# Performance work log

Hardware: AMD Instinct MI355X
Metric: run time of the kernel (lower is better)

Reference implementation:

```python
import jax, jax.numpy as jnp
import numpy as np

B, S, E = 2, 2048, 2048
H, KVH, D = 16, 4, 128
GROUPS = H // KVH
WINDOW = 1024
CAP = 50.0
ROPE_BASE = 10000.0
RMS_EPS = 1e-6
LN_EPS = 1e-5

def setup_inputs() -> dict:
    key = jax.random.key(0)
    ks = jax.random.split(key, 5)
    return {
        "x": jax.random.normal(ks[0], (B, S, E), jnp.float32),
        "Wq": jax.random.normal(ks[1], (E, E), jnp.float32) * (1.0 / np.sqrt(E)),
        "Wk": jax.random.normal(ks[2], (KVH * D, E), jnp.float32) * (1.0 / np.sqrt(E)),
        "Wv": jax.random.normal(ks[3], (KVH * D, E), jnp.float32) * (1.0 / np.sqrt(E)),
        "Wo": jax.random.normal(ks[4], (E, E), jnp.float32) * (1.0 / np.sqrt(E * H)),
        "q_norm_w": jnp.ones((D,), jnp.float32),
        "k_norm_w": jnp.ones((D,), jnp.float32),
        "ln_gamma": jnp.ones((E,), jnp.float32),
        "ln_beta": jnp.zeros((E,), jnp.float32),
    }

def _rmsnorm(t, w):
    # normalize over last (head) dim
    var = jnp.mean(jnp.square(t), axis=-1, keepdims=True)
    return t * jax.lax.rsqrt(var + RMS_EPS) * w

def _rope(t):
    # t: [B, h, S, D]; rotate-half RoPE
    half = D // 2
    inv_freq = 1.0 / (ROPE_BASE ** (jnp.arange(0, D, 2, dtype=jnp.float32) / D))  # [D/2]
    ang = jnp.arange(S, dtype=jnp.float32)[:, None] * inv_freq[None, :]  # [S, D/2]
    cos = jnp.concatenate([jnp.cos(ang), jnp.cos(ang)], axis=-1)  # [S, D]
    sin = jnp.concatenate([jnp.sin(ang), jnp.sin(ang)], axis=-1)
    t1, t2 = t[..., :half], t[..., half:]
    rot = jnp.concatenate([-t2, t1], axis=-1)
    return t * cos + rot * sin

def reference(x, Wq, Wk, Wv, Wo, q_norm_w, k_norm_w, ln_gamma, ln_beta):
    b, s, _ = x.shape
    q = (x @ Wq.T).reshape(b, s, H, D).transpose(0, 2, 1, 3)    # [B,H,S,D]
    k = (x @ Wk.T).reshape(b, s, KVH, D).transpose(0, 2, 1, 3)  # [B,KVH,S,D]
    v = (x @ Wv.T).reshape(b, s, KVH, D).transpose(0, 2, 1, 3)
    # QK-RMSNorm (Gemma/PaLM2 style), then RoPE
    q = _rope(_rmsnorm(q, q_norm_w))
    k = _rope(_rmsnorm(k, k_norm_w))
    # GQA: repeat KV heads to match query heads
    k = jnp.repeat(k, GROUPS, axis=1)  # [B,H,S,D]
    v = jnp.repeat(v, GROUPS, axis=1)
    scores = jnp.einsum('bhqd,bhkd->bhqk', q, k) / jnp.sqrt(jnp.asarray(D, x.dtype))
    # tanh logit softcap (Gemma2)
    scores = CAP * jnp.tanh(scores / CAP)
    # causal + sliding-window mask: attend to j with 0 <= i-j < WINDOW
    i = jnp.arange(s)[:, None]
    j = jnp.arange(s)[None, :]
    mask = (j <= i) & ((i - j) < WINDOW)  # [S,S]
    neg = jnp.finfo(scores.dtype).min
    scores = jnp.where(mask[None, None], scores, neg)
    attn = jax.nn.softmax(scores, axis=-1)
    out = jnp.einsum('bhqk,bhkd->bhqd', attn, v)  # [B,H,S,D]
    out = out.transpose(0, 2, 1, 3).reshape(b, s, E) @ Wo.T
    # residual + LayerNorm (post-norm)
    y = x + out
    mu = jnp.mean(y, axis=-1, keepdims=True)
    var = jnp.var(y, axis=-1, keepdims=True)
    return (y - mu) * jax.lax.rsqrt(var + LN_EPS) * ln_gamma + ln_beta
```

## Files before the change

kernel.cpp:

```cpp
#include <hip/hip_runtime.h>
#include <stdint.h>

typedef __attribute__((ext_vector_type(8))) short short8;
typedef __attribute__((ext_vector_type(4))) float f32x4;
typedef unsigned short u16;
typedef unsigned int u32;

#define NTOK 4096
#define E 2048
#define S 2048
#define NH 16
#define NKVH 4
#define HD 128
#define NQKV 3072

__device__ __forceinline__ float bf2f(u16 u) {
    return __uint_as_float(((u32)u) << 16);
}
__device__ __forceinline__ u16 f2bf(float f) {
    u32 u = __float_as_uint(f);
    u32 r = (u + 0x7fffu + ((u >> 16) & 1u)) >> 16;
    return (u16)r;
}
__device__ __forceinline__ void gload_lds16(const u16* g, u16* l) {
    __builtin_amdgcn_global_load_lds(
        (const __attribute__((address_space(1))) unsigned int*)(g),
        (__attribute__((address_space(3))) unsigned int*)(l), 16, 0, 0);
}

__global__ void cast5(const float* __restrict__ x, const float* __restrict__ wq,
                      const float* __restrict__ wk, const float* __restrict__ wv,
                      const float* __restrict__ wo,
                      u16* __restrict__ xb, u16* __restrict__ wqkvb,
                      u16* __restrict__ wob) {
    int i = blockIdx.x * 256 + threadIdx.x;
    const float* s; u16* d; int rel;
    if (i < 2097152)      { s = x;  d = xb;  rel = i; }
    else if (i < 3145728) { s = wq; d = wqkvb; rel = i - 2097152; }
    else if (i < 3407872) { s = wk; d = wqkvb + 4194304; rel = i - 3145728; }
    else if (i < 3670016) { s = wv; d = wqkvb + 5242880; rel = i - 3407872; }
    else                  { s = wo; d = wob; rel = i - 3670016; }
    float4 v = *(const float4*)(s + (size_t)rel * 4);
    ushort4 o;
    o.x = f2bf(v.x); o.y = f2bf(v.y); o.z = f2bf(v.z); o.w = f2bf(v.w);
    *(ushort4*)(d + (size_t)rel * 4) = o;
}

#define LADDR(row, ko) ((row) * 64 + ((ko) ^ (((row) & 7) << 3)))
#define GSB   __builtin_amdgcn_sched_barrier(0)
#define GBAR  __builtin_amdgcn_s_barrier()
#define LGKM0 do { asm volatile("s_waitcnt lgkmcnt(0)" ::: "memory"); GSB; } while (0)
#define MIDBAR do { GSB; GBAR; LGKM0; } while (0)
#define ENDBAR do { __builtin_amdgcn_s_setprio(0); GSB; GBAR; } while (0)

__device__ __forceinline__ void stage1(u16* lds, const u16* g, int row0,
                                       int kt, int K, int tid) {
    const int rr = tid >> 3;
    const int chunk = (tid & 7) ^ (rr & 7);
    gload_lds16(g + (size_t)(row0 + rr) * K + kt + chunk * 8,
                lds + (row0 + (tid >> 6) * 8) * 64);
}

__global__ __launch_bounds__(512, 2)
void gemm_qkv(const u16* __restrict__ A, const u16* __restrict__ Bt,
              float* __restrict__ C, int M, int N, int K) {
    __shared__ u16 As2[2 * 8192];
    __shared__ u16 Bs2[2 * 24576];
    const int tid = threadIdx.x;
    const int w = tid >> 6, lane = tid & 63;
    const int lr = lane & 15, quad = lane >> 4;
    const int qo = quad * 8;
    const int wr = w >> 2, wc = w & 3;
    const int am = wr * 64;
    const int bn = wc * 96;

    const int nbx = N / 384;
    int wg = blockIdx.x;
    {
        const int nwg = gridDim.x;
        const int q = nwg >> 3, r = nwg & 7;
        const int xcd = wg & 7, loc = wg >> 3;
        wg = (xcd < r ? xcd * (q + 1) : r * (q + 1) + (xcd - r) * q) + loc;
    }
    const int n0 = (wg % nbx) * 384;
    const int m0 = (wg / nbx) * 128;

    const u16* gA = A + (size_t)m0 * K;
    const u16* gB = Bt + (size_t)n0 * K;
    const int nt = K >> 6;

    f32x4 acc[4][6];
#pragma unroll
    for (int mi = 0; mi < 4; mi++)
#pragma unroll
        for (int ni = 0; ni < 6; ni++)
            acc[mi][ni] = (f32x4){0.f, 0.f, 0.f, 0.f};

    short8 af[4][2], bf[6][2];

    stage1(As2, gA, 0, 0, K, tid);
    stage1(As2, gA, 64, 0, K, tid);
#pragma unroll
    for (int r = 0; r < 6; r++) stage1(Bs2, gB, r * 64, 0, K, tid);
    if (nt > 1) {
        stage1(As2 + 8192, gA, 0, 64, K, tid);
        stage1(As2 + 8192, gA, 64, 64, K, tid);
#pragma unroll
        for (int r = 0; r < 4; r++) stage1(Bs2 + 24576, gB, r * 64, 64, K, tid);
        asm volatile("s_waitcnt vmcnt(6)" ::: "memory");
    } else {
        asm volatile("s_waitcnt vmcnt(0)" ::: "memory");
    }
    GSB; GBAR;

    for (int t = 0; t < nt; ++t) {
        const int pb = t & 1;
        u16* Ap = As2 + pb * 8192;
        u16* Bp = Bs2 + pb * 24576;
        u16* Bn = Bs2 + (pb ^ 1) * 24576;
        const int kt1 = (t + 1) << 6, kt2 = (t + 2) << 6;

#pragma unroll
        for (int mi = 0; mi < 4; mi++)
#pragma unroll
            for (int kk = 0; kk < 2; kk++)
                af[mi][kk] = *(const short8*)&Ap[LADDR(am + mi * 16 + lr, kk * 32 + qo)];
#pragma unroll
        for (int ni = 0; ni < 3; ni++)
#pragma unroll
            for (int kk = 0; kk < 2; kk++)
                bf[ni][kk] = *(const short8*)&Bp[LADDR(bn + ni * 16 + lr, kk * 32 + qo)];
        if (t + 1 < nt) {
            stage1(Bn, gB, 256, kt1, K, tid);
            stage1(Bn, gB, 320, kt1, K, tid);
        }
        MIDBAR;
        __builtin_amdgcn_s_setprio(1);
#pragma unroll
        for (int mi = 0; mi < 2; mi++)
#pragma unroll
            for (int ni = 0; ni < 3; ni++)
#pragma unroll
                for (int kk = 0; kk < 2; kk++)
                    acc[mi][ni] = __builtin_amdgcn_mfma_f32_16x16x32_bf16(
                        af[mi][kk], bf[ni][kk], acc[mi][ni], 0, 0, 0);
        ENDBAR;

#pragma unroll
        for (int ni = 3; ni < 6; ni++)
#pragma unroll
            for (int kk = 0; kk < 2; kk++)
                bf[ni][kk] = *(const short8*)&Bp[LADDR(bn + ni * 16 + lr, kk * 32 + qo)];
        if (t + 2 < nt) {
            stage1(Ap, gA, 0, kt2, K, tid);
            stage1(Ap, gA, 64, kt2, K, tid);
        }
        MIDBAR;
        __builtin_amdgcn_s_setprio(1);
#pragma unroll
        for (int mi = 0; mi < 2; mi++)
#pragma unroll
            for (int ni = 3; ni < 6; ni++)
#pragma unroll
                for (int kk = 0; kk < 2; kk++)
                    acc[mi][ni] = __builtin_amdgcn_mfma_f32_16x16x32_bf16(
                        af[mi][kk], bf[ni][kk], acc[mi][ni], 0, 0, 0);
        ENDBAR;

        if (t + 2 < nt) {
#pragma unroll
            for (int r = 0; r < 4; r++) stage1(Bp, gB, r * 64, kt2, K, tid);
        }
        __builtin_amdgcn_s_setprio(1);
#pragma unroll
        for (int mi = 2; mi < 4; mi++)
#pragma unroll
            for (int ni = 0; ni < 6; ni++)
#pragma unroll
                for (int kk = 0; kk < 2; kk++)
                    acc[mi][ni] = __builtin_amdgcn_mfma_f32_16x16x32_bf16(
                        af[mi][kk], bf[ni][kk], acc[mi][ni], 0, 0, 0);
        __builtin_amdgcn_s_setprio(0);
        if (t + 2 >= nt) {
            asm volatile("s_waitcnt vmcnt(0)" ::: "memory");
        } else {
            asm volatile("s_waitcnt vmcnt(6)" ::: "memory");
        }
        GSB; GBAR;
    }

#pragma unroll
    for (int mi = 0; mi < 4; mi++)
#pragma unroll
        for (int ni = 0; ni < 6; ni++) {
            const int row = m0 + am + mi * 16 + quad * 4;
            const int col = n0 + bn + ni * 16 + lr;
            f32x4 v = acc[mi][ni];
            C[(size_t)(row + 0) * N + col] = v[0];
            C[(size_t)(row + 1) * N + col] = v[1];
            C[(size_t)(row + 2) * N + col] = v[2];
            C[(size_t)(row + 3) * N + col] = v[3];
        }
}

__device__ __forceinline__ void stageA(u16* lds, const u16* g, int ldsrow0,
                                       int g0, int g1, int kt, int K, int tid) {
    const int rr = tid >> 3;
    const int chunk = (tid & 7) ^ (rr & 7);
    const int w8 = (tid >> 6) * 8;
    gload_lds16(g + (size_t)(g0 + rr) * K + kt + chunk * 8,
                lds + (ldsrow0 + w8) * 64);
    gload_lds16(g + (size_t)(g1 + rr) * K + kt + chunk * 8,
                lds + (ldsrow0 + 64 + w8) * 64);
}
__device__ __forceinline__ void stageB(u16* lds, const u16* g, int ldsrow0,
                                       int b0, int b1, int kt, int K, int tid) {
    const int rr = tid >> 3;
    const int grow = (rr & 31) | ((rr & 32) << 1);
    const int chunk = (tid & 7) ^ (rr & 7);
    const int w8 = (tid >> 6) * 8;
    gload_lds16(g + (size_t)(b0 + grow) * K + kt + chunk * 8,
                lds + (ldsrow0 + w8) * 64);
    gload_lds16(g + (size_t)(b1 + grow) * K + kt + chunk * 8,
                lds + (ldsrow0 + 64 + w8) * 64);
}

__global__ __launch_bounds__(512, 2)
void gemm8p(const u16* __restrict__ A, const u16* __restrict__ Bt,
            float* __restrict__ C, int M, int N, int K, int ksz, int nsplit) {
    __shared__ u16 As[2 * 16384];
    __shared__ u16 Bs[2 * 16384];
    const int tid = threadIdx.x;
    const int w = tid >> 6, lane = tid & 63;
    const int lr = lane & 15, quad = lane >> 4;
    const int qo = quad * 8;
    const int wm = (w >> 2) * 128, wn = (w & 3) * 64;
    const int wmh = (w >> 2) * 64, wnq = (w & 3) * 32;

    const int nbx = N >> 8;
    int wg = blockIdx.x;
    {
        const int nwg = gridDim.x;
        const int q = nwg >> 3, r = nwg & 7;
        const int xcd = wg & 7, loc = wg >> 3;
        wg = (xcd < r ? xcd * (q + 1) : r * (q + 1) + (xcd - r) * q) + loc;
    }
    int split = 0;
    if (nsplit == 2) { split = wg & 1; wg >>= 1; }
    const int n0 = (wg % nbx) << 8;
    const int m0 = (wg / nbx) << 8;

    const u16* gA = A + (size_t)m0 * K + split * ksz;
    const u16* gB = Bt + (size_t)n0 * K + split * ksz;
    C += (size_t)split * M * N;
    const int nt = ksz >> 6;

    f32x4 acc[8][4];
#pragma unroll
    for (int mi = 0; mi < 8; mi++)
#pragma unroll
        for (int ni = 0; ni < 4; ni++)
            acc[mi][ni] = (f32x4){0.f, 0.f, 0.f, 0.f};

    short8 alo[4][2], ahi[4][2], blo[2][2], bhi[2][2];

    stageA(As, gA, 0, 0, 128, 0, K, tid);
    stageB(Bs, gB, 0, 0, 128, 0, K, tid);
    stageB(Bs, gB, 128, 32, 160, 0, K, tid);
    stageA(As, gA, 128, 64, 192, 0, K, tid);
    if (nt > 1) {
        stageA(As + 16384, gA, 0, 0, 128, 64, K, tid);
        stageB(Bs + 16384, gB, 0, 0, 128, 64, K, tid);
        stageB(Bs + 16384, gB, 128, 32, 160, 64, K, tid);
        asm volatile("s_waitcnt vmcnt(6)" ::: "memory");
    } else {
        asm volatile("s_waitcnt vmcnt(0)" ::: "memory");
    }
    GSB; GBAR;

    for (int t = 0; t < nt; ++t) {
        const int pb = t & 1;
        u16* Ap = As + pb * 16384;
        u16* Bp = Bs + pb * 16384;
        u16* An = As + (pb ^ 1) * 16384;
        const int kt1 = (t + 1) << 6, kt2 = (t + 2) << 6;

#pragma unroll
        for (int mi = 0; mi < 4; mi++)
#pragma unroll
            for (int kk = 0; kk < 2; kk++)
                alo[mi][kk] = *(const short8*)&Ap[LADDR(wmh + mi * 16 + lr, kk * 32 + qo)];
#pragma unroll
        for (int ni = 0; ni < 2; ni++)
#pragma unroll
            for (int kk = 0; kk < 2; kk++)
                blo[ni][kk] = *(const short8*)&Bp[LADDR(wnq + ni * 16 + lr, kk * 32 + qo)];
        if (t + 1 < nt) stageA(An, gA, 128, 64, 192, kt1, K, tid);
        MIDBAR;
        __builtin_amdgcn_s_setprio(1);
#pragma unroll
        for (int mi = 0; mi < 4; mi++)
#pragma unroll
            for (int ni = 0; ni < 2; ni++)
#pragma unroll
                for (int kk = 0; kk < 2; kk++)
                    acc[mi][ni] = __builtin_amdgcn_mfma_f32_16x16x32_bf16(
                        alo[mi][kk], blo[ni][kk], acc[mi][ni], 0, 0, 0);
        ENDBAR;

#pragma unroll
        for (int ni = 0; ni < 2; ni++)
#pragma unroll
            for (int kk = 0; kk < 2; kk++)
                bhi[ni][kk] = *(const short8*)&Bp[LADDR(128 + wnq + ni * 16 + lr, kk * 32 + qo)];
        if (t + 2 < nt) stageA(Ap, gA, 0, 0, 128, kt2, K, tid);
        MIDBAR;
        __builtin_amdgcn_s_setprio(1);
#pragma unroll
        for (int mi = 0; mi < 4; mi++)
#pragma unroll
            for (int ni = 0; ni < 2; ni++)
#pragma unroll
                for (int kk = 0; kk < 2; kk++)
                    acc[mi][ni + 2] = __builtin_amdgcn_mfma_f32_16x16x32_bf16(
                        alo[mi][kk], bhi[ni][kk], acc[mi][ni + 2], 0, 0, 0);
        ENDBAR;

#pragma unroll
        for (int mi = 0; mi < 4; mi++)
#pragma unroll
            for (int kk = 0; kk < 2; kk++)
                ahi[mi][kk] = *(const short8*)&Ap[LADDR(128 + wmh + mi * 16 + lr, kk * 32 + qo)];
        if (t + 2 < nt) stageB(Bp, gB, 0, 0, 128, kt2, K, tid);
        MIDBAR;
        __builtin_amdgcn_s_setprio(1);
#pragma unroll
        for (int mi = 0; mi < 4; mi++)
#pragma unroll
            for (int ni = 0; ni < 2; ni++)
#pragma unroll
                for (int kk = 0; kk < 2; kk++)
                    acc[mi + 4][ni + 2] = __builtin_amdgcn_mfma_f32_16x16x32_bf16(
                        ahi[mi][kk], bhi[ni][kk], acc[mi + 4][ni + 2], 0, 0, 0);
        ENDBAR;

        if (t + 2 < nt) stageB(Bp, gB, 128, 32, 160, kt2, K, tid);
        __builtin_amdgcn_s_setprio(1);
#pragma unroll
        for (int mi = 0; mi < 4; mi++)
#pragma unroll
            for (int ni = 0; ni < 2; ni++)
#pragma unroll
                for (int kk = 0; kk < 2; kk++)
                    acc[mi + 4][ni] = __builtin_amdgcn_mfma_f32_16x16x32_bf16(
                        ahi[mi][kk], blo[ni][kk], acc[mi + 4][ni], 0, 0, 0);
        __builtin_amdgcn_s_setprio(0);
        if (t + 2 >= nt) {
            asm volatile("s_waitcnt vmcnt(0)" ::: "memory");
        } else {
            asm volatile("s_waitcnt vmcnt(6)" ::: "memory");
        }
        GSB; GBAR;
    }

#pragma unroll
    for (int mi = 0; mi < 8; mi++)
#pragma unroll
        for (int ni = 0; ni < 4; ni++) {
            const int row = m0 + wm + mi * 16 + quad * 4;
            const int col = n0 + wn + ni * 16 + lr;
            f32x4 v = acc[mi][ni];
            C[(size_t)(row + 0) * N + col] = v[0];
            C[(size_t)(row + 1) * N + col] = v[1];
            C[(size_t)(row + 2) * N + col] = v[2];
            C[(size_t)(row + 3) * N + col] = v[3];
        }
}

#define LDT 65
#define RMSBLKS 20480
__global__ __launch_bounds__(256)
void prep(const float* __restrict__ qkv,
          const float* __restrict__ qw, const float* __restrict__ kw,
          u16* __restrict__ qdst, u16* __restrict__ kdst, u16* __restrict__ vdst) {
    __shared__ u16 Ts[128 * LDT];
    if (blockIdx.x < RMSBLKS) {
        int p = blockIdx.x * 4 + (threadIdx.x >> 6);
        int lane = threadIdx.x & 63;
        const float* src; const float* w; u16* dst; int HH;
        if (p < NTOK * NH) { src = qkv; w = qw; dst = qdst; HH = NH; }
        else { p -= NTOK * NH; src = qkv + 2048; w = kw; dst = kdst; HH = NKVH; }
        int n = p / HH;
        int h = p - n * HH;
        int b = n >> 11;
        int s = n & 2047;
        const float* row = src + (size_t)n * NQKV + h * HD;
        float t1 = row[lane];
        float t2 = row[lane + 64];
        float ss = t1 * t1 + t2 * t2;
#pragma unroll
        for (int o = 1; o < 64; o <<= 1) ss += __shfl_xor(ss, o);
        float r = rsqrtf(ss * (1.f / 128.f) + 1e-6f);
        float a1 = t1 * r * w[lane];
        float a2 = t2 * r * w[lane + 64];
        float freq = expf(lane * -0.14391156831212787f);
        float ang = (float)s * freq;
        float sn, cs;
        sincosf(ang, &sn, &cs);
        float o1 = a1 * cs - a2 * sn;
        float o2 = a2 * cs + a1 * sn;
        size_t base = (((size_t)(b * HH + h)) * S + s) * HD;
        dst[base + lane] = f2bf(o1);
        dst[base + 64 + lane] = f2bf(o2);
    } else {
        const int idx = blockIdx.x - RMSBLKS;
        const int t = threadIdx.x;
        const int s0 = (idx & 31) * 64;
        const int kh = (idx >> 5) & 3;
        const int b = idx >> 7;
        const float* base = qkv + ((size_t)(b * S + s0)) * NQKV + 2560 + kh * HD;
#pragma unroll
        for (int i = 0; i < 8; i++) {
            int ii = i * 256 + t;
            int r = ii >> 5, c4 = (ii & 31) * 4;
            float4 v = *(const float4*)(base + (size_t)r * NQKV + c4);
            Ts[(c4 + 0) * LDT + r] = f2bf(v.x);
            Ts[(c4 + 1) * LDT + r] = f2bf(v.y);
            Ts[(c4 + 2) * LDT + r] = f2bf(v.z);
            Ts[(c4 + 3) * LDT + r] = f2bf(v.w);
        }
        __syncthreads();
        u16* obase = vdst + ((size_t)(b * NKVH + kh) * HD) * S + s0;
#pragma unroll
        for (int i = 0; i < 4; i++) {
            int ii = i * 256 + t;
            int d = ii >> 3, s8 = (ii & 7) * 8;
            const u16* row = &Ts[d * LDT + s8];
            short8 o;
#pragma unroll
            for (int j = 0; j < 8; j++) o[j] = (short)row[j];
            *(short8*)(obase + (size_t)d * S + s8) = o;
        }
    }
}

#define KSX(key, cb) ((key) * 128 + ((((cb) ^ ((key) & 15))) * 8))
#define VSX(d, cb)   ((d) * 64 + ((((cb) ^ ((d) & 7))) * 8))
#define PSX(row, cb) ((row) * 64 + ((((cb) ^ ((row) & 7))) * 8))
#define QBLK 64

__global__ __launch_bounds__(256, 4)
void attn_mfma(const u16* __restrict__ qa, const u16* __restrict__ ka,
               const u16* __restrict__ vt, u16* __restrict__ out) {
    __shared__ u16 Ks[64 * 128];
    __shared__ u16 Vs[128 * 64];
    __shared__ u16 Ps[64 * 64];
    const int tid = threadIdx.x;
    const int w = tid >> 6, lane = tid & 63;
    const int lr = lane & 15, quad = lane >> 4;
    const int hb = blockIdx.x;
    const int h = hb >> 1, b = hb & 1;
    const int kh = h >> 2;
    const int qt = (int)(gridDim.y - 1) - blockIdx.y;
    const int q0 = qt * QBLK;
    const int qg0 = q0 + w * 16;

    const float KQK = 0.0051006974f;
    const float KP  = -144.26950408889634f;

    short8 qf[4];
    {
        const u16* qrow = qa + (((size_t)(b * NH + h)) * S + qg0 + lr) * HD;
#pragma unroll
        for (int c = 0; c < 4; c++)
            qf[c] = *(const short8*)(qrow + c * 32 + quad * 8);
    }

    f32x4 O[8];
#pragma unroll
    for (int dt = 0; dt < 8; dt++) O[dt] = (f32x4){0.f, 0.f, 0.f, 0.f};
    float l[4] = {0.f, 0.f, 0.f, 0.f};

    const u16* kbase0 = ka + (((size_t)(b * NKVH + kh)) * S) * HD;
    const u16* vtbase0 = vt + ((size_t)(b * NKVH + kh) * HD) * S;

    const int jt0 = (q0 >= 1024) ? (q0 - 1024) : 0;
    const int jtend = q0;
    const int qmin = qg0, qmax = qg0 + 15;

    for (int jt = jt0; jt <= jtend; jt += 64) {
        const u16* kbase = kbase0 + (size_t)jt * HD;
        const u16* vtbase = vtbase0 + jt;
        __syncthreads();
#pragma unroll
        for (int i = 0; i < 4; i++) {
            int idx = i * 256 + tid;
            int key = idx >> 4, cbk = (idx & 15) ^ (key & 15);
            gload_lds16(kbase + (size_t)key * HD + cbk * 8,
                        &Ks[(i * 256 + w * 64) * 8]);
            int dd = idx >> 3, cbv = (idx & 7) ^ (dd & 7);
            gload_lds16(vtbase + (size_t)dd * S + cbv * 8,
                        &Vs[(i * 256 + w * 64) * 8]);
        }
        __syncthreads();

        u16* Pw = &Ps[w * 16 * 64];
        bool any = false;

#pragma unroll
        for (int kt = 0; kt < 4; kt++) {
            const int keymin = jt + kt * 16;
            bool need = (keymin <= qmax) && (keymin + 15 >= qmin - 1023);
            bool full = (keymin + 15 <= qmin) && (keymin >= qmax - 1023);
            if (need) {
                any = true;
                f32x4 a = (f32x4){0.f, 0.f, 0.f, 0.f};
#pragma unroll
                for (int c = 0; c < 4; c++) {
                    short8 kf = *(const short8*)(&Ks[KSX(kt * 16 + lr, 4 * c + quad)]);
                    a = __builtin_amdgcn_mfma_f32_16x16x32_bf16(qf[c], kf, a, 0, 0, 0);
                }
#pragma unroll
                for (int r = 0; r < 4; r++) {
                    float t = __builtin_amdgcn_exp2f(a[r] * KQK);
                    float p = __builtin_amdgcn_exp2f(
                        KP * __builtin_amdgcn_rcpf(t + 1.f));
                    if (!full) {
                        int rel = keymin + lr - (qg0 + quad * 4 + r);
                        bool valid = (rel <= 0) && (rel > -1024);
                        p = valid ? p : 0.f;
                    }
                    l[r] += p;
                    Pw[PSX(quad * 4 + r, kt * 2 + (lr >> 3)) + (lr & 7)] =
                        (u16)(__float_as_uint(p) >> 16);
                }
            } else {
#pragma unroll
                for (int r = 0; r < 4; r++)
                    Pw[PSX(quad * 4 + r, kt * 2 + (lr >> 3)) + (lr & 7)] = 0;
            }
        }

        if (any) {
#pragma unroll
            for (int c2 = 0; c2 < 2; c2++) {
                short8 pf = *(const short8*)(&Pw[PSX(lr, c2 * 4 + quad)]);
#pragma unroll
                for (int dt = 0; dt < 8; dt++) {
                    short8 vf = *(const short8*)(&Vs[VSX(dt * 16 + lr, c2 * 4 + quad)]);
                    O[dt] = __builtin_amdgcn_mfma_f32_16x16x32_bf16(pf, vf, O[dt], 0, 0, 0);
                }
            }
        }
    }

#pragma unroll
    for (int r = 0; r < 4; r++) {
        l[r] += __shfl_xor(l[r], 1);
        l[r] += __shfl_xor(l[r], 2);
        l[r] += __shfl_xor(l[r], 4);
        l[r] += __shfl_xor(l[r], 8);
    }
#pragma unroll
    for (int r = 0; r < 4; r++) {
        float inv = 1.f / l[r];
        u16* orow = out + ((size_t)(b * S + qg0 + quad * 4 + r)) * E + h * HD;
#pragma unroll
        for (int dt = 0; dt < 8; dt++)
            orow[dt * 16 + lr] = f2bf(O[dt][r] * inv);
    }
}

__global__ __launch_bounds__(256)
void ln_kernel(const float* __restrict__ x, const float* __restrict__ pr,
               const float* __restrict__ pr2,
               const float* __restrict__ g, const float* __restrict__ be,
               float* __restrict__ out) {
    int n = blockIdx.x;
    int tid = threadIdx.x;
    const float* xr = x + (size_t)n * E;
    const float* p = pr + (size_t)n * E;
    const float* p2 = pr2 + (size_t)n * E;
    float y[8];
    float s = 0.f, ss = 0.f;
#pragma unroll
    for (int i = 0; i < 2; i++) {
        float4 a = *(const float4*)(xr + tid * 8 + i * 4);
        float4 b = *(const float4*)(p + tid * 8 + i * 4);
        float4 cc = *(const float4*)(p2 + tid * 8 + i * 4);
        float v0 = a.x + b.x + cc.x, v1 = a.y + b.y + cc.y;
        float v2 = a.z + b.z + cc.z, v3 = a.w + b.w + cc.w;
        y[i * 4 + 0] = v0; y[i * 4 + 1] = v1; y[i * 4 + 2] = v2; y[i * 4 + 3] = v3;
        s += v0 + v1 + v2 + v3;
        ss += v0 * v0 + v1 * v1 + v2 * v2 + v3 * v3;
    }
#pragma unroll
    for (int o = 1; o < 64; o <<= 1) {
        s += __shfl_xor(s, o);
        ss += __shfl_xor(ss, o);
    }
    __shared__ float r0[4], r1[4];
    int w = tid >> 6;
    if ((tid & 63) == 0) { r0[w] = s; r1[w] = ss; }
    __syncthreads();
    s = r0[0] + r0[1] + r0[2] + r0[3];
    ss = r1[0] + r1[1] + r1[2] + r1[3];
    float mu = s * (1.f / 2048.f);
    float var = ss * (1.f / 2048.f) - mu * mu;
    float rs = rsqrtf(var + 1e-5f);
    float* orow = out + (size_t)n * E;
#pragma unroll
    for (int i = 0; i < 8; i++) {
        int c = tid * 8 + i;
        orow[c] = (y[i] - mu) * rs * g[c] + be[c];
    }
}

extern "C" void kernel_launch(void* const* d_in, const int* in_sizes, int n_in,
                              void* d_out, int out_size, void* d_ws, size_t ws_size,
                              hipStream_t stream) {
    (void)in_sizes; (void)n_in; (void)out_size; (void)ws_size;
    const float* x   = (const float*)d_in[0];
    const float* Wq  = (const float*)d_in[1];
    const float* Wk  = (const float*)d_in[2];
    const float* Wv  = (const float*)d_in[3];
    const float* Wo  = (const float*)d_in[4];
    const float* qnw = (const float*)d_in[5];
    const float* knw = (const float*)d_in[6];
    const float* lng = (const float*)d_in[7];
    const float* lnb = (const float*)d_in[8];
    float* out = (float*)d_out;

    char* ws = (char*)d_ws;
    size_t off = 0;
    auto alloc = [&](size_t bytes) -> char* {
        char* pp = ws + off;
        off = (off + bytes + 255) & ~(size_t)255;
        return pp;
    };
    u16*  xb     = (u16*)alloc((size_t)NTOK * E * 2);
    u16*  Wqkvb  = (u16*)alloc((size_t)NQKV * E * 2);
    u16*  Wob    = (u16*)alloc((size_t)E * E * 2);
    float* qkvraw= (float*)alloc((size_t)NTOK * NQKV * 4);
    u16*  qaa    = (u16*)alloc((size_t)NTOK * E * 2);
    u16*  kaa    = (u16*)alloc((size_t)NTOK * 512 * 2);
    u16*  vtt    = (u16*)alloc((size_t)NTOK * 512 * 2);
    u16*  attn_o = xb;
    float* proj  = qkvraw;

    cast5<<<dim3(18432), 256, 0, stream>>>(x, Wq, Wk, Wv, Wo, xb, Wqkvb, Wob);

    gemm_qkv<<<dim3(256), 512, 0, stream>>>(xb, Wqkvb, qkvraw, NTOK, NQKV, E);

    prep<<<dim3(RMSBLKS + 256), 256, 0, stream>>>(qkvraw, qnw, knw, qaa, kaa, vtt);

    attn_mfma<<<dim3(NH * 2, S / QBLK), 256, 0, stream>>>(qaa, kaa, vtt, attn_o);

    gemm8p<<<dim3((NTOK / 256) * (E / 256) * 2), 512, 0, stream>>>(
        attn_o, Wob, proj, NTOK, E, E, E / 2, 2);

    ln_kernel<<<dim3(NTOK), 256, 0, stream>>>(
        x, proj, proj + (size_t)NTOK * E, lng, lnb, out);
}
```

Before: 308.9 us.

## Double-buffer K/V tiles in sliding-window attention to overlap loads with MFMA

The attention kernel now keeps two LDS buffers each for K and V. It prefetches the next key tile's K and V while the current tile's QK^T, softcap and PV MFMAs run. Explicit vmcnt waits and barriers separate K readiness from V readiness, so the QK phase only waits on K. This hides global-to-LDS load latency, but it nearly doubles LDS use and lowers launch bounds from 4 to 2 blocks per CU, so there is less occupancy left to hide latency.

```diff
diff --git a/kernel.cpp b/kernel.cpp
--- a/kernel.cpp
+++ b/kernel.cpp
@@ -449,11 +449,28 @@
 #define PSX(row, cb) ((row) * 64 + ((((cb) ^ ((row) & 7))) * 8))
 #define QBLK 64
 
-__global__ __launch_bounds__(256, 4)
+__device__ __forceinline__ void stageKtile(u16* dstK, const u16* kbase, int tid, int w) {
+#pragma unroll
+    for (int i = 0; i < 4; i++) {
+        int idx = i * 256 + tid;
+        int key = idx >> 4, cbk = (idx & 15) ^ (key & 15);
+        gload_lds16(kbase + (size_t)key * HD + cbk * 8, dstK + (i * 256 + w * 64) * 8);
+    }
+}
+__device__ __forceinline__ void stageVtile(u16* dstV, const u16* vtbase, int tid, int w) {
+#pragma unroll
+    for (int i = 0; i < 4; i++) {
+        int idx = i * 256 + tid;
+        int dd = idx >> 3, cbv = (idx & 7) ^ (dd & 7);
+        gload_lds16(vtbase + (size_t)dd * S + cbv * 8, dstV + (i * 256 + w * 64) * 8);
+    }
+}
+
+__global__ __launch_bounds__(256, 2)
 void attn_mfma(const u16* __restrict__ qa, const u16* __restrict__ ka,
                const u16* __restrict__ vt, u16* __restrict__ out) {
-    __shared__ u16 Ks[64 * 128];
-    __shared__ u16 Vs[128 * 64];
+    __shared__ u16 Ks[2][64 * 128];
+    __shared__ u16 Vs[2][128 * 64];
     __shared__ u16 Ps[64 * 64];
     const int tid = threadIdx.x;
     const int w = tid >> 6, lane = tid & 63;
@@ -488,23 +505,21 @@
     const int jtend = q0;
     const int qmin = qg0, qmax = qg0 + 15;
 
+    stageKtile(Ks[0], kbase0 + (size_t)jt0 * HD, tid, w);
+    stageVtile(Vs[0], vtbase0 + jt0, tid, w);
+    asm volatile("s_waitcnt vmcnt(4)" ::: "memory");
+    GSB; GBAR;
+
     for (int jt = jt0; jt <= jtend; jt += 64) {
-        const u16* kbase = kbase0 + (size_t)jt * HD;
-        const u16* vtbase = vtbase0 + jt;
-        __syncthreads();
-#pragma unroll
-        for (int i = 0; i < 4; i++) {
-            int idx = i * 256 + tid;
-            int key = idx >> 4, cbk = (idx & 15) ^ (key & 15);
-            gload_lds16(kbase + (size_t)key * HD + cbk * 8,
-                        &Ks[(i * 256 + w * 64) * 8]);
-            int dd = idx >> 3, cbv = (idx & 7) ^ (dd & 7);
-            gload_lds16(vtbase + (size_t)dd * S + cbv * 8,
-                        &Vs[(i * 256 + w * 64) * 8]);
-        }
-        __syncthreads();
+        const int cur = ((jt - jt0) >> 6) & 1;
+        const bool hasnext = (jt + 64 <= jtend);
+        if (hasnext) {
+            stageKtile(Ks[cur ^ 1], kbase0 + (size_t)(jt + 64) * HD, tid, w);
+            stageVtile(Vs[cur ^ 1], vtbase0 + (jt + 64), tid, w);
+        }
 
         u16* Pw = &Ps[w * 16 * 64];
+        const u16* Kc = Ks[cur];
         bool any = false;
 
 #pragma unroll
@@ -517,7 +532,7 @@
                 f32x4 a = (f32x4){0.f, 0.f, 0.f, 0.f};
 #pragma unroll
                 for (int c = 0; c < 4; c++) {
-                    short8 kf = *(const short8*)(&Ks[KSX(kt * 16 + lr, 4 * c + quad)]);
+                    short8 kf = *(const short8*)(&Kc[KSX(kt * 16 + lr, 4 * c + quad)]);
                     a = __builtin_amdgcn_mfma_f32_16x16x32_bf16(qf[c], kf, a, 0, 0, 0);
                 }
 #pragma unroll
@@ -541,17 +556,28 @@
             }
         }
 
+        if (hasnext) {
+            asm volatile("s_waitcnt vmcnt(8)" ::: "memory");
+        } else {
+            asm volatile("s_waitcnt vmcnt(0)" ::: "memory");
+        }
+        GSB; GBAR;
+
         if (any) {
+            const u16* Vc = Vs[cur];
 #pragma unroll
             for (int c2 = 0; c2 < 2; c2++) {
                 short8 pf = *(const short8*)(&Pw[PSX(lr, c2 * 4 + quad)]);
 #pragma unroll
                 for (int dt = 0; dt < 8; dt++) {
-                    short8 vf = *(const short8*)(&Vs[VSX(dt * 16 + lr, c2 * 4 + quad)]);
+                    short8 vf = *(const short8*)(&Vc[VSX(dt * 16 + lr, c2 * 4 + quad)]);
                     O[dt] = __builtin_amdgcn_mfma_f32_16x16x32_bf16(pf, vf, O[dt], 0, 0, 0);
                 }
             }
         }
+
+        asm volatile("s_waitcnt vmcnt(4)" ::: "memory");
+        GSB; GBAR;
     }
 
 #pragma unroll
```

Result: slower. 323.3 us (+4.7%).
